# Performance work log

Measured on AMD Instinct MI355X. Metric: run time of the kernel, lower is better.

The kernel has to match this reference:

```python
import jax, jax.numpy as jnp
import numpy as np

B, T, I, H = 4096, 2048, 4, 3


def setup_inputs() -> dict:
    key = jax.random.key(0)
    ks = jax.random.split(key, 6)
    input_seq = jax.random.normal(ks[0], (B, T, I), dtype=jnp.float32)
    # pack_padded_sequence(enforce_sorted=True) requires descending lengths; max == T
    length = jnp.sort(jax.random.randint(ks[1], (B,), 1, T + 1))[::-1]
    length = length.at[0].set(T).astype(jnp.int64)
    s = 0.1
    W_ih = jax.random.normal(ks[2], (4 * H, I), dtype=jnp.float32) * s  # gate order: i,f,g,o
    W_hh = jax.random.normal(ks[3], (4 * H, H), dtype=jnp.float32) * s
    b_ih = jax.random.normal(ks[4], (4 * H,), dtype=jnp.float32) * s
    b_hh = jax.random.normal(ks[5], (4 * H,), dtype=jnp.float32) * s
    return {"input_seq": input_seq, "W_ih": W_ih, "W_hh": W_hh,
            "b_ih": b_ih, "b_hh": b_hh, "length": length}


def _lstm_padded(input_seq, W_ih, W_hh, b_ih, b_hh, length):
    # Precompute input projections for all timesteps: [B,T,4H]
    x_proj = jnp.einsum('bti,gi->btg', input_seq, W_ih) + (b_ih + b_hh)
    x_proj_t = jnp.swapaxes(x_proj, 0, 1)  # [T,B,4H]

    def step(carry, xg):
        h, c = carry
        gates = xg + h @ W_hh.T  # [B,4H]
        i, f, g, o = jnp.split(gates, 4, axis=-1)
        i = jax.nn.sigmoid(i)
        f = jax.nn.sigmoid(f)
        g = jnp.tanh(g)
        o = jax.nn.sigmoid(o)
        c = f * c + i * g
        h = o * jnp.tanh(c)
        return (h, c), h

    h0 = jnp.zeros((B, H), dtype=input_seq.dtype)
    c0 = jnp.zeros((B, H), dtype=input_seq.dtype)
    _, hs = jax.lax.scan(step, (h0, c0), x_proj_t)  # hs: [T,B,H]
    hs = jnp.swapaxes(hs, 0, 1)  # [B,T,H]
    # pad_packed_sequence zeros out positions t >= length; valid prefix is unaffected
    mask = (jnp.arange(T)[None, :] < length[:, None])[..., None]
    return jnp.where(mask, hs, 0.0)


def reference(input_seq, W_ih, W_hh, b_ih, b_hh, length):
    return _lstm_padded(input_seq, W_ih, W_hh, b_ih, b_hh, length)
```

## Files before the change

### kernel.cpp

```cpp
#include <hip/hip_runtime.h>


#define BB 4096
#define TT 2048
#define L2E 1.4426950408889634f

template<int CTRL>
__device__ __forceinline__ float dppf(float v) {
    return __int_as_float(
        __builtin_amdgcn_update_dpp(0, __float_as_int(v), CTRL, 0xF, 0xF, true));
}

__global__ __launch_bounds__(64, 1) void lstm_seq(
    const float* __restrict__ x, const float* __restrict__ Wih,
    const float* __restrict__ Whh, const float* __restrict__ bih,
    const float* __restrict__ bhh, const int* __restrict__ len,
    float* __restrict__ out)
{
    const int lane  = threadIdx.x & 63;
    const int s     = lane & 3;
    const int q     = (lane >> 2) & 3;
    const int row16 = lane >> 4;
    const int b     = blockIdx.x * 4 + row16;
    const int u     = (q < 3) ? q : 2;
    const int wrow  = s * 3 + u;

    const float scale = (s == 2) ? (2.f * L2E) : (-L2E);
    const float Aa = (s == 2) ? (2.f * L2E) : 0.f;
    const float Bb = (s == 2) ? (-4.f * L2E) : 1.f;

    const float xw0 = Wih[wrow * 4 + 0] * scale;
    const float xw1 = Wih[wrow * 4 + 1] * scale;
    const float xw2 = Wih[wrow * 4 + 2] * scale;
    const float xw3 = Wih[wrow * 4 + 3] * scale;
    const float bias = (bih[wrow] + bhh[wrow]) * scale;

    float wh[4];
    #pragma unroll
    for (int j = 0; j < 4; ++j) {
        const int srcq = (q - j) & 3;
        wh[j] = (srcq == 3) ? 0.f : Whh[wrow * 3 + srcq] * scale;
    }

    const int mylen = len[b];
    int wmax = mylen;
    #pragma unroll
    for (int off = 1; off < 64; off <<= 1)
        wmax = max(wmax, __shfl_xor(wmax, off));
    const int Tloop = (wmax + 7) & ~7;

    float myh = 0.f, cc = 0.f;
    const float4* __restrict__ xrow = ((const float4*)x) + (size_t)b * TT;
    float* __restrict__ orow = out + (size_t)b * (TT * 3);
    const bool writer = (s == 0) && (q < 3);

    float4 buf[8];
    float xacc[8];
    #pragma unroll
    for (int uu = 0; uu < 8; ++uu) buf[uu] = xrow[uu];

    for (int tb = 0; tb < Tloop; tb += 8) {
        #pragma unroll
        for (int uu = 0; uu < 8; ++uu) {
            const float4 xv = buf[uu];
            xacc[uu] = fmaf(xw3, xv.w, fmaf(xw2, xv.z,
                       fmaf(xw1, xv.y, fmaf(xw0, xv.x, bias))));
        }
        #pragma unroll
        for (int uu = 0; uu < 8; ++uu) {
            const int tn = tb + 8 + uu;
            buf[uu] = xrow[tn < TT ? tn : 0];
        }
        #pragma unroll
        for (int uu = 0; uu < 8; ++uu) {
            const int t = tb + uu;
            const float h1 = dppf<0x124>(myh);
            const float h2 = dppf<0x128>(myh);
            const float h3 = dppf<0x12C>(myh);
            const float p0 = fmaf(wh[0], myh, xacc[uu]);
            const float m3 = wh[3] * h3;
            const float p1 = fmaf(wh[1], h1, p0);
            const float p2 = fmaf(wh[2], h2, m3);
            const float a  = p1 + p2;
            const float r = __builtin_amdgcn_rcpf(1.f + __builtin_amdgcn_exp2f(a));
            const float act = fmaf(Bb, r, Aa);
            const float gi = dppf<0x00>(act);
            const float gf = dppf<0x55>(act);
            const float gg = dppf<0xAA>(act);
            const float go = dppf<0xFF>(act);
            cc = fmaf(gf, cc, gi * gg);
            const float n2go = -2.f * go;
            const float r2 = __builtin_amdgcn_rcpf(1.f + __builtin_amdgcn_exp2f(cc));
            myh = fmaf(n2go, r2, go);
            if (writer) orow[t * 3 + q] = myh;
        }
    }

    asm volatile("s_waitcnt vmcnt(0)" ::: "memory");

    #pragma unroll
    for (int rr = 0; rr < 4; ++rr) {
        const int bb = blockIdx.x * 4 + rr;
        const int L  = len[bb];
        float* __restrict__ ob = out + (size_t)bb * (TT * 3);
        const int s0 = L * 3;
        const int a4 = (s0 + 3) & ~3;
        if (lane < a4 - s0) ob[s0 + lane] = 0.f;
        float4* __restrict__ o4 = (float4*)ob;
        for (int idx = a4 / 4 + lane; idx < TT * 3 / 4; idx += 64)
            o4[idx] = make_float4(0.f, 0.f, 0.f, 0.f);
    }
}

extern "C" void kernel_launch(void* const* d_in, const int* in_sizes, int n_in,
                              void* d_out, int out_size, void* d_ws, size_t ws_size,
                              hipStream_t stream) {
    const float* x    = (const float*)d_in[0];
    const float* Wih  = (const float*)d_in[1];
    const float* Whh  = (const float*)d_in[2];
    const float* bih  = (const float*)d_in[3];
    const float* bhh  = (const float*)d_in[4];
    const int*   lenp = (const int*)d_in[5];
    float* out = (float*)d_out;

    lstm_seq<<<BB / 4, 64, 0, stream>>>(x, Wih, Whh, bih, bhh, lenp, out);
}
```

Measured before the change: 407.3 us.

## Refactor LSTM recurrence to shorten critical path via algebraic split of h

Writes h = go - 2*go*r2 and precomputes the go-dependent part of the next step's recurrent matmul (S1, D coefficients) off the critical path. The next pre-activation then depends only on r2 through one DPP+FMA chain, instead of waiting for the full h. The input-projection prefetch is restructured so the next step's x term is available early. Output stores are batched per 8-step chunk. This adds extra DPP and multiply work per step and changes floating-point rounding order slightly.

```diff
diff --git a/kernel.cpp b/kernel.cpp
--- a/kernel.cpp
+++ b/kernel.cpp
@@ -49,19 +49,27 @@
         wmax = max(wmax, __shfl_xor(wmax, off));
     const int Tloop = (wmax + 7) & ~7;
 
-    float myh = 0.f, cc = 0.f;
     const float4* __restrict__ xrow = ((const float4*)x) + (size_t)b * TT;
     float* __restrict__ orow = out + (size_t)b * (TT * 3);
     const bool writer = (s == 0) && (q < 3);
 
     float4 buf[8];
-    float xacc[8];
     #pragma unroll
     for (int uu = 0; uu < 8; ++uu) buf[uu] = xrow[uu];
 
+    float cc = 0.f, r2p = 0.f, go = 0.f;
+    float D0 = 0.f, D1 = 0.f, D2 = 0.f, D3 = 0.f;
+    float S1;
+    {
+        const float4 xv = buf[0];
+        S1 = fmaf(xw3, xv.w, fmaf(xw2, xv.z,
+             fmaf(xw1, xv.y, fmaf(xw0, xv.x, bias))));
+    }
+
     for (int tb = 0; tb < Tloop; tb += 8) {
+        float xacc[8];
         #pragma unroll
-        for (int uu = 0; uu < 8; ++uu) {
+        for (int uu = 1; uu < 8; ++uu) {
             const float4 xv = buf[uu];
             xacc[uu] = fmaf(xw3, xv.w, fmaf(xw2, xv.z,
                        fmaf(xw1, xv.y, fmaf(xw0, xv.x, bias))));
@@ -71,28 +79,51 @@
             const int tn = tb + 8 + uu;
             buf[uu] = xrow[tn < TT ? tn : 0];
         }
+        float msave[8];
         #pragma unroll
         for (int uu = 0; uu < 8; ++uu) {
-            const int t = tb + uu;
-            const float h1 = dppf<0x124>(myh);
-            const float h2 = dppf<0x128>(myh);
-            const float h3 = dppf<0x12C>(myh);
-            const float p0 = fmaf(wh[0], myh, xacc[uu]);
-            const float m3 = wh[3] * h3;
-            const float p1 = fmaf(wh[1], h1, p0);
-            const float p2 = fmaf(wh[2], h2, m3);
-            const float a  = p1 + p2;
-            const float r = __builtin_amdgcn_rcpf(1.f + __builtin_amdgcn_exp2f(a));
+            const float R1 = dppf<0x124>(r2p);
+            const float R2 = dppf<0x128>(r2p);
+            const float R3 = dppf<0x12C>(r2p);
+            const float e0  = fmaf(D0, r2p, S1);
+            const float u01 = fmaf(D1, R1, e0);
+            const float m2v = D2 * R2;
+            const float u23 = fmaf(D3, R3, m2v);
+            const float a   = u01 + u23;
+            const float r   = __builtin_amdgcn_rcpf(1.f + __builtin_amdgcn_exp2f(a));
             const float act = fmaf(Bb, r, Aa);
             const float gi = dppf<0x00>(act);
             const float gf = dppf<0x55>(act);
             const float gg = dppf<0xAA>(act);
-            const float go = dppf<0xFF>(act);
+            go = dppf<0xFF>(act);
             cc = fmaf(gf, cc, gi * gg);
+            const float e2 = __builtin_amdgcn_exp2f(cc);
+            const float G1 = dppf<0x124>(go);
+            const float G2 = dppf<0x128>(go);
+            const float G3 = dppf<0x12C>(go);
+            const float P0 = wh[0] * go;
+            const float P1 = wh[1] * G1;
+            const float P2 = wh[2] * G2;
+            const float P3 = wh[3] * G3;
+            float xn;
+            if (uu < 7) {
+                xn = xacc[uu + 1];
+            } else {
+                const float4 xv = buf[0];
+                xn = fmaf(xw3, xv.w, fmaf(xw2, xv.z,
+                     fmaf(xw1, xv.y, fmaf(xw0, xv.x, bias))));
+            }
+            S1 = xn + ((P0 + P1) + (P2 + P3));
+            D0 = -2.f * P0; D1 = -2.f * P1; D2 = -2.f * P2; D3 = -2.f * P3;
             const float n2go = -2.f * go;
-            const float r2 = __builtin_amdgcn_rcpf(1.f + __builtin_amdgcn_exp2f(cc));
-            myh = fmaf(n2go, r2, go);
-            if (writer) orow[t * 3 + q] = myh;
+            const float r2 = __builtin_amdgcn_rcpf(1.f + e2);
+            msave[uu] = fmaf(n2go, r2, go);
+            r2p = r2;
+        }
+        if (writer) {
+            #pragma unroll
+            for (int uu = 0; uu < 8; ++uu)
+                orow[(tb + uu) * 3 + q] = msave[uu];
         }
     }
 
```

After: 444.3 us. +9.1%, slower.
